# Performance work log

Hardware: AMD Instinct MI355X
Metric: run time of the kernel (lower is better)

## Reference

```python
import jax, jax.numpy as jnp
import numpy as np
import math

NO, NR, E = 100000, 1000, 1000000
DO, DR, DE, H, OM = 64, 32, 4, 64, 32


def setup_inputs() -> dict:
    key = jax.random.key(0)
    ks = jax.random.split(key, 20)
    s = lambda k, sh: jax.random.normal(k, sh, dtype=jnp.float32) * 0.05
    inp = {
        'x_order': jax.random.normal(ks[0], (NO, DO), dtype=jnp.float32),
        'x_rider': jax.random.normal(ks[1], (NR, DR), dtype=jnp.float32),
        'edge_attr': jax.random.normal(ks[2], (E, DE), dtype=jnp.float32),
        'order_idx': jax.random.randint(ks[3], (E,), 0, NO),
        'rider_idx': jax.random.randint(ks[4], (E,), 0, NR),
        'omega_encoded': jax.random.normal(ks[5], (OM,), dtype=jnp.float32),
        # TransformerConv params (heads=1)
        'Wk': s(ks[6], (DO, H)), 'bk': jnp.zeros((H,), jnp.float32),
        'Wq': s(ks[7], (DR, H)), 'bq': jnp.zeros((H,), jnp.float32),
        'Wv': s(ks[8], (DO, H)), 'bv': jnp.zeros((H,), jnp.float32),
        'We': s(ks[9], (DE, H)),  # lin_edge, bias=False in PyG
        'Wskip': s(ks[10], (DR, H)), 'bskip': jnp.zeros((H,), jnp.float32),
        # order_proj
        'Wp': s(ks[11], (DO, H)), 'bp': jnp.zeros((H,), jnp.float32),
        # residual MLP: Linear(2H+OM,128) -> ReLU -> Linear(128,1)
        'W1': s(ks[12], (2 * H + OM, 128)), 'b1': jnp.zeros((128,), jnp.float32),
        'W2': s(ks[13], (128, 1)), 'b2': jnp.zeros((1,), jnp.float32),
    }
    return inp


def _segment_softmax(alpha, seg, num_segments):
    m = jax.ops.segment_max(alpha, seg, num_segments=num_segments)
    m = jnp.where(jnp.isfinite(m), m, 0.0)
    ex = jnp.exp(alpha - m[seg])
    denom = jax.ops.segment_sum(ex, seg, num_segments=num_segments)
    return ex / (denom[seg] + 1e-16)


def reference(x_order, x_rider, edge_attr, order_idx, rider_idx, omega_encoded,
              Wk, bk, Wq, bq, Wv, bv, We, Wskip, bskip, Wp, bp, W1, b1, W2, b2):
    scale = 1.0 / math.sqrt(H)
    # TransformerConv((order, rider) -> rider), heads=1, edge_dim
    q = x_rider @ Wq + bq            # [NR, H]
    k = x_order @ Wk + bk            # [NO, H]
    v = x_order @ Wv + bv            # [NO, H]
    e = edge_attr @ We               # [E, H]
    k_j = k[order_idx] + e           # [E, H]
    v_j = v[order_idx] + e           # [E, H]
    alpha = jnp.sum(q[rider_idx] * k_j, axis=-1) * scale  # [E]
    alpha = _segment_softmax(alpha, rider_idx, NR)
    agg = jax.ops.segment_sum(alpha[:, None] * v_j, rider_idx, num_segments=NR)  # [NR, H]
    rider_emb = agg + x_rider @ Wskip + bskip  # root/skip connection

    # edge scoring
    order_proj = x_order @ Wp + bp   # [NO, H]
    oe = order_proj[order_idx]       # [E, H]
    re = rider_emb[rider_idx]        # [E, H]
    dot = jnp.sum(oe * re, axis=-1) * scale  # [E]
    omega_expand = jnp.broadcast_to(omega_encoded[None, :], (oe.shape[0], OM))
    resid_in = jnp.concatenate([oe, re, omega_expand], axis=-1)  # [E, 2H+OM]
    hmid = jax.nn.relu(resid_in @ W1 + b1)
    resid = (hmid @ W2 + b2)[:, 0]
    return jnp.clip(dot + resid, -10.0, 10.0)
```

## Files before the change

### kernel.cpp

```cpp
#include <hip/hip_runtime.h>
#include <hip/hip_bf16.h>
#include <math.h>
#include <stdint.h>

#define NO_N 100000
#define NR_N 1000
#define E_N  1000000
#define SB     250
#define SCHUNK 4000
#define KVP_TILES 1563
#define KVP_BLKS 1024
#define MAXTILES 17008

typedef short bf16x8 __attribute__((ext_vector_type(8)));
typedef float floatx4 __attribute__((ext_vector_type(4)));

__device__ __forceinline__ unsigned short bfu(float x) {
    union { __hip_bfloat16 h; unsigned short u; } c;
    c.h = __float2bfloat16(x);
    return c.u;
}
__device__ __forceinline__ float bflo(unsigned int u) {
    return __uint_as_float(u << 16);
}
__device__ __forceinline__ float bfhi(unsigned int u) {
    return __uint_as_float(u & 0xffff0000u);
}

__global__ __launch_bounds__(256) void k_front(
    const float* __restrict__ xr,
    const float* __restrict__ Wq, const float* __restrict__ bq,
    const float* __restrict__ Wskip, const float* __restrict__ bskip,
    const float* __restrict__ We,
    float* __restrict__ q, float* __restrict__ skip, float* __restrict__ t,
    const float* __restrict__ W1, const float* __restrict__ b1,
    const float* __restrict__ omega, float* __restrict__ b1eff,
    unsigned short* __restrict__ w1t,
    const float* __restrict__ x,
    const float* __restrict__ Wk, const float* __restrict__ bk,
    const float* __restrict__ Wv, const float* __restrict__ bv,
    const float* __restrict__ Wp, const float* __restrict__ bp,
    unsigned short* __restrict__ kb, unsigned short* __restrict__ vb,
    unsigned short* __restrict__ pb,
    const int* __restrict__ ridx, int* __restrict__ ghist)
{
    __shared__ __align__(16) char smem[9216];
    const int tid = threadIdx.x;
    const int b = blockIdx.x;

    if (b < 250) {
        float* sx = (float*)smem;
        float* sq = sx + 128;
        int rbase = b * 4;
        if (tid < 128) {
            int rl = tid >> 5, d = tid & 31;
            sx[rl * 32 + d] = xr[(rbase + rl) * 32 + d];
        }
        __syncthreads();
        int rl = tid >> 6, h = tid & 63;
        int r = rbase + rl;
        float aq = bq[h], as = bskip[h];
        #pragma unroll 4
        for (int d = 0; d < 32; ++d) {
            float xv = sx[rl * 32 + d];
            aq += xv * Wq[d * 64 + h];
            as += xv * Wskip[d * 64 + h];
        }
        sq[rl * 64 + h] = aq;
        q[r * 64 + h] = aq;
        skip[r * 64 + h] = as;
        __syncthreads();
        if (tid < 16) {
            int rl2 = tid >> 2, d = tid & 3;
            float acc = 0.f;
            for (int hh = 0; hh < 64; ++hh)
                acc += We[d * 64 + hh] * sq[rl2 * 64 + hh];
            t[(rbase + rl2) * 4 + d] = acc;
        }
    } else if (b == 250) {
        if (tid < 128) {
            float acc = b1[tid];
            #pragma unroll 4
            for (int j = 0; j < 32; ++j)
                acc += omega[j] * W1[(128 + j) * 128 + tid];
            b1eff[tid] = acc;
        }
        for (int idx = tid; idx < 64 * 128; idx += 256) {
            int n = idx >> 6, k = idx & 63;
            w1t[idx] = bfu(W1[k * 128 + n]);
        }
    } else if (b < 251 + KVP_BLKS) {
        unsigned short* sX = (unsigned short*)smem;
        const int wave = tid >> 6, lane = tid & 63;
        const int l15 = lane & 15, quad = lane >> 4;

        bf16x8 bfr[3][2];
        float bias[3];
        unsigned short* outT[3];
        int colc[3];
        #pragma unroll
        for (int ct = 0; ct < 3; ++ct) {
            int n = wave * 48 + ct * 16 + l15;
            int table = n >> 6, c = n & 63;
            const float* W  = (table == 0) ? Wk : (table == 1) ? Wv : Wp;
            const float* bb = (table == 0) ? bk : (table == 1) ? bv : bp;
            bias[ct] = bb[c];
            colc[ct] = c;
            outT[ct] = (table == 0) ? kb : (table == 1) ? vb : pb;
            #pragma unroll
            for (int kf = 0; kf < 2; ++kf) {
                bf16x8 f;
                #pragma unroll
                for (int j = 0; j < 8; ++j)
                    f[j] = (short)bfu(W[(size_t)(kf * 32 + quad * 8 + j) * 64 + c]);
                bfr[ct][kf] = f;
            }
        }

        const int srl = tid >> 2;
        const int sqt = (tid & 3) * 16;

        for (int tile = b - 251; tile < KVP_TILES; tile += KVP_BLKS) {
            int rowbase = tile * 64;
            {
                int row = rowbase + srl;
                unsigned short* dst = sX + srl * 72 + sqt;
                if (row < NO_N) {
                    const float4* src = (const float4*)(x + (size_t)row * 64 + sqt);
                    #pragma unroll
                    for (int i = 0; i < 4; ++i) {
                        float4 a = src[i];
                        ushort4 u = { bfu(a.x), bfu(a.y), bfu(a.z), bfu(a.w) };
                        *(ushort4*)(dst + i * 4) = u;
                    }
                } else {
                    ushort4 z = {0, 0, 0, 0};
                    #pragma unroll
                    for (int i = 0; i < 4; ++i) *(ushort4*)(dst + i * 4) = z;
                }
            }
            __syncthreads();

            floatx4 acc[4][3];
            #pragma unroll
            for (int rt = 0; rt < 4; ++rt)
                #pragma unroll
                for (int ct = 0; ct < 3; ++ct)
                    acc[rt][ct] = (floatx4){bias[ct], bias[ct], bias[ct], bias[ct]};

            #pragma unroll
            for (int rt = 0; rt < 4; ++rt) {
                const unsigned short* ar = sX + (size_t)(rt * 16 + l15) * 72 + quad * 8;
                bf16x8 a0 = *(const bf16x8*)(ar);
                bf16x8 a1 = *(const bf16x8*)(ar + 32);
                #pragma unroll
                for (int ct = 0; ct < 3; ++ct) {
                    floatx4 c = acc[rt][ct];
                    c = __builtin_amdgcn_mfma_f32_16x16x32_bf16(a0, bfr[ct][0], c, 0, 0, 0);
                    c = __builtin_amdgcn_mfma_f32_16x16x32_bf16(a1, bfr[ct][1], c, 0, 0, 0);
                    acc[rt][ct] = c;
                }
            }

            #pragma unroll
            for (int rt = 0; rt < 4; ++rt) {
                int rb = rowbase + rt * 16 + quad * 4;
                #pragma unroll
                for (int ct = 0; ct < 3; ++ct) {
                    unsigned short* o = outT[ct];
                    size_t cbase = colc[ct];
                    #pragma unroll
                    for (int g = 0; g < 4; ++g) {
                        int row = rb + g;
                        if (row < NO_N)
                            o[(size_t)row * 64 + cbase] = bfu(acc[rt][ct][g]);
                    }
                }
            }
            __syncthreads();
        }
    } else {
        int* hc = (int*)smem;
        int hb = b - (251 + KVP_BLKS);
        for (int i = tid; i < NR_N; i += 256) hc[i] = 0;
        __syncthreads();
        int s = hb * SCHUNK;
        for (int i = s + tid; i < s + SCHUNK; i += 256)
            atomicAdd(&hc[ridx[i]], 1);
        __syncthreads();
        for (int i = tid; i < NR_N; i += 256)
            ghist[i * SB + hb] = hc[i];
    }
}

__global__ __launch_bounds__(256) void k_colscan(const int* __restrict__ ghist,
                                                 int* __restrict__ gpre,
                                                 int* __restrict__ counts)
{
    __shared__ int s[256];
    int tid = threadIdx.x, r = blockIdx.x;
    int v = (tid < SB) ? ghist[r * SB + tid] : 0;
    s[tid] = v;
    __syncthreads();
    for (int off = 1; off < 256; off <<= 1) {
        int tv = (tid >= off) ? s[tid - off] : 0;
        __syncthreads();
        s[tid] += tv;
        __syncthreads();
    }
    if (tid < SB) gpre[r * SB + tid] = s[tid] - v;
    if (tid == 255) counts[r] = s[255];
}

__global__ __launch_bounds__(1024) void k_scan(const int* __restrict__ counts,
                                               int* __restrict__ offsets,
                                               int* __restrict__ tilestart)
{
    __shared__ int s[1024];
    int tid = threadIdx.x;
    int c = (tid < NR_N) ? counts[tid] : 0;
    s[tid] = c;
    __syncthreads();
    for (int off = 1; off < 1024; off <<= 1) {
        int tv = (tid >= off) ? s[tid - off] : 0;
        __syncthreads();
        s[tid] += tv;
        __syncthreads();
    }
    if (tid < NR_N) offsets[tid] = s[tid] - c;
    if (tid == NR_N - 1) offsets[NR_N] = s[tid];
    __syncthreads();
    int tc = (tid < NR_N) ? ((c + 63) >> 6) : 0;
    s[tid] = tc;
    __syncthreads();
    for (int off = 1; off < 1024; off <<= 1) {
        int tv = (tid >= off) ? s[tid - off] : 0;
        __syncthreads();
        s[tid] += tv;
        __syncthreads();
    }
    if (tid < NR_N) tilestart[tid] = s[tid] - tc;
    if (tid == NR_N - 1) tilestart[NR_N] = s[tid];
}

__global__ __launch_bounds__(256) void k_trec(const int* __restrict__ tilestart,
                                              const int* __restrict__ offsets,
                                              int4* __restrict__ trec)
{
    int nt = tilestart[NR_N];
    int t = blockIdx.x * 256 + threadIdx.x;
    if (t >= nt) return;
    int lo = 0, hi = NR_N - 1;
    while (lo < hi) {
        int mid = (lo + hi + 1) >> 1;
        if (tilestart[mid] <= t) lo = mid; else hi = mid - 1;
    }
    trec[t] = make_int4(lo, offsets[lo] + ((t - tilestart[lo]) << 6),
                        offsets[lo + 1], 0);
}

__global__ __launch_bounds__(1024) void k_scatter2(
    const int* __restrict__ ridx, const int* __restrict__ oidx,
    const float* __restrict__ ea, const float* __restrict__ t,
    const int* __restrict__ offsets, const int* __restrict__ gpre,
    int4* __restrict__ spack, int* __restrict__ so, int* __restrict__ rank)
{
    __shared__ int cur[NR_N];
    int tid = threadIdx.x, b = blockIdx.x;
    for (int i = tid; i < NR_N; i += 1024)
        cur[i] = offsets[i] + gpre[i * SB + b];
    __syncthreads();
    int s = b * SCHUNK;
    for (int i = s + tid; i < s + SCHUNK; i += 1024) {
        int r = ridx[i];
        int o = oidx[i];
        float4 e4 = *(const float4*)(ea + (size_t)i * 4);
        float4 t4 = *(const float4*)(t + r * 4);
        float h = e4.x * t4.x + e4.y * t4.y + e4.z * t4.z + e4.w * t4.w;
        int pos = atomicAdd(&cur[r], 1);
        int4 pk;
        pk.x = o;
        pk.y = __float_as_int(h);
        pk.z = (int)((unsigned)bfu(e4.x) | ((unsigned)bfu(e4.y) << 16));
        pk.w = (int)((unsigned)bfu(e4.z) | ((unsigned)bfu(e4.w) << 16));
        spack[pos] = pk;
        so[pos] = o;
        rank[i] = pos;
    }
}

__global__ __launch_bounds__(512) void k_rider(
    const int* __restrict__ offsets, const int4* __restrict__ spack,
    const float* __restrict__ q,
    const unsigned short* __restrict__ kb, const unsigned short* __restrict__ vb,
    const float* __restrict__ We, const float* __restrict__ skip,
    const float* __restrict__ W1, const float* __restrict__ b1eff,
    unsigned short* __restrict__ embb, float* __restrict__ Br)
{
    __shared__ float sQ[64];
    __shared__ int2 sOX[8][64];
    __shared__ float rv[8][64];
    __shared__ float re4[8][4];
    __shared__ float rd[8];

    int r = blockIdx.x;
    int wave = threadIdx.x >> 6, lane = threadIdx.x & 63;
    if (threadIdx.x < 64) sQ[threadIdx.x] = q[r * 64 + threadIdx.x];
    __syncthreads();

    int beg = offsets[r], end = offsets[r + 1];
    int cnt = end - beg;
    int chunk = (cnt + 7) >> 3;
    int s0 = beg + wave * chunk;
    int s1 = min(s0 + chunk, end);

    float aggv = 0.f, dsum = 0.f;
    float ag0 = 0.f, ag1 = 0.f, ag2 = 0.f, ag3 = 0.f;
    const float2* sQ2 = (const float2*)sQ;

    for (int jb = s0; jb < s1; jb += 64) {
        int j = jb + lane;
        bool valid = (j < s1);
        int4 pk = make_int4(0, 0, 0, 0);
        if (valid) pk = spack[j];
        int oo = pk.x;
        float h = __int_as_float(pk.y);

        const uint4* krow = (const uint4*)(kb + (size_t)oo * 64);
        uint4 K0 = krow[0], K1 = krow[1], K2 = krow[2], K3 = krow[3];
        uint4 K4 = krow[4], K5 = krow[5], K6 = krow[6], K7 = krow[7];
        float acc = h;
        #define DOT8(Kv, base) { \
            float2 qa = sQ2[(base) + 0]; \
            acc = fmaf(bflo(Kv.x), qa.x, acc); acc = fmaf(bfhi(Kv.x), qa.y, acc); \
            float2 qb = sQ2[(base) + 1]; \
            acc = fmaf(bflo(Kv.y), qb.x, acc); acc = fmaf(bfhi(Kv.y), qb.y, acc); \
            float2 qc = sQ2[(base) + 2]; \
            acc = fmaf(bflo(Kv.z), qc.x, acc); acc = fmaf(bfhi(Kv.z), qc.y, acc); \
            float2 qd = sQ2[(base) + 3]; \
            acc = fmaf(bflo(Kv.w), qd.x, acc); acc = fmaf(bfhi(Kv.w), qd.y, acc); }
        DOT8(K0, 0) DOT8(K1, 4) DOT8(K2, 8) DOT8(K3, 12)
        DOT8(K4, 16) DOT8(K5, 20) DOT8(K6, 24) DOT8(K7, 28)
        #undef DOT8

        float exv = valid ? __expf(acc * 0.125f) : 0.f;
        dsum += exv;
        unsigned int ez = (unsigned int)pk.z, ew = (unsigned int)pk.w;
        ag0 = fmaf(exv, bflo(ez), ag0);
        ag1 = fmaf(exv, bfhi(ez), ag1);
        ag2 = fmaf(exv, bflo(ew), ag2);
        ag3 = fmaf(exv, bfhi(ew), ag3);

        sOX[wave][lane] = make_int2(oo, __float_as_int(exv));

        int nn = min(s1 - jb, 64);
        int i = 0;
        for (; i + 8 <= nn; i += 8) {
            int2 x0 = sOX[wave][i + 0], x1 = sOX[wave][i + 1];
            int2 x2 = sOX[wave][i + 2], x3 = sOX[wave][i + 3];
            int2 x4 = sOX[wave][i + 4], x5 = sOX[wave][i + 5];
            int2 x6 = sOX[wave][i + 6], x7 = sOX[wave][i + 7];
            unsigned short u0 = vb[(size_t)x0.x * 64 + lane];
            unsigned short u1 = vb[(size_t)x1.x * 64 + lane];
            unsigned short u2 = vb[(size_t)x2.x * 64 + lane];
            unsigned short u3 = vb[(size_t)x3.x * 64 + lane];
            unsigned short u4 = vb[(size_t)x4.x * 64 + lane];
            unsigned short u5 = vb[(size_t)x5.x * 64 + lane];
            unsigned short u6 = vb[(size_t)x6.x * 64 + lane];
            unsigned short u7 = vb[(size_t)x7.x * 64 + lane];
            aggv = fmaf(__int_as_float(x0.y), __uint_as_float((unsigned int)u0 << 16), aggv);
            aggv = fmaf(__int_as_float(x1.y), __uint_as_float((unsigned int)u1 << 16), aggv);
            aggv = fmaf(__int_as_float(x2.y), __uint_as_float((unsigned int)u2 << 16), aggv);
            aggv = fmaf(__int_as_float(x3.y), __uint_as_float((unsigned int)u3 << 16), aggv);
            aggv = fmaf(__int_as_float(x4.y), __uint_as_float((unsigned int)u4 << 16), aggv);
            aggv = fmaf(__int_as_float(x5.y), __uint_as_float((unsigned int)u5 << 16), aggv);
            aggv = fmaf(__int_as_float(x6.y), __uint_as_float((unsigned int)u6 << 16), aggv);
            aggv = fmaf(__int_as_float(x7.y), __uint_as_float((unsigned int)u7 << 16), aggv);
        }
        for (; i < nn; ++i) {
            int2 xx = sOX[wave][i];
            unsigned short uu = vb[(size_t)xx.x * 64 + lane];
            aggv = fmaf(__int_as_float(xx.y), __uint_as_float((unsigned int)uu << 16), aggv);
        }
    }

    #pragma unroll
    for (int m = 1; m < 64; m <<= 1) {
        dsum += __shfl_xor(dsum, m);
        ag0 += __shfl_xor(ag0, m);
        ag1 += __shfl_xor(ag1, m);
        ag2 += __shfl_xor(ag2, m);
        ag3 += __shfl_xor(ag3, m);
    }

    rv[wave][lane] = aggv;
    if (lane == 0) {
        rd[wave] = dsum;
        re4[wave][0] = ag0; re4[wave][1] = ag1;
        re4[wave][2] = ag2; re4[wave][3] = ag3;
    }
    __syncthreads();
    if (threadIdx.x < 64) {
        int l = threadIdx.x;
        float av = 0.f, ds = 0.f, a0 = 0.f, a1 = 0.f, a2 = 0.f, a3 = 0.f;
        #pragma unroll
        for (int w = 0; w < 8; ++w) {
            av += rv[w][l]; ds += rd[w];
            a0 += re4[w][0]; a1 += re4[w][1]; a2 += re4[w][2]; a3 += re4[w][3];
        }
        float corr = a0 * We[0 * 64 + l] + a1 * We[1 * 64 + l]
                   + a2 * We[2 * 64 + l] + a3 * We[3 * 64 + l];
        float val = (av + corr) / (ds + 1e-16f) + skip[r * 64 + l];
        embb[r * 64 + l] = bfu(val);
        sQ[l] = val;
    }
    __syncthreads();
    if (threadIdx.x < 128) {
        int c = threadIdx.x;
        float a = b1eff[c];
        #pragma unroll 8
        for (int d = 0; d < 64; ++d)
            a = fmaf(sQ[d], W1[(size_t)(64 + d) * 128 + c], a);
        Br[r * 128 + c] = a;
    }
}

__global__ __launch_bounds__(256) void k_edge2(
    const int* __restrict__ so, const int4* __restrict__ trec,
    const int* __restrict__ tilestart,
    const unsigned short* __restrict__ pb, const unsigned short* __restrict__ embb,
    const float* __restrict__ Br, const unsigned short* __restrict__ w1t,
    const float* __restrict__ W2, const float* __restrict__ b2,
    float* __restrict__ tmp)
{
    const int tid = threadIdx.x;
    const int wave = tid >> 6;
    const int lane = tid & 63;
    const int l15 = lane & 15;
    const int quad = lane >> 4;

    bf16x8 bfr[8][2];
    floatx4 w2q[8];
    #pragma unroll
    for (int ctl = 0; ctl < 8; ++ctl) {
        int n = ctl * 16 + l15;
        bfr[ctl][0] = *(const bf16x8*)(w1t + n * 64 + quad * 8);
        bfr[ctl][1] = *(const bf16x8*)(w1t + n * 64 + 32 + quad * 8);
        w2q[ctl] = *(const floatx4*)(W2 + ctl * 16 + quad * 4);
    }
    float b2v = b2[0];
    const int ntiles = tilestart[NR_N];
    const bf16x8 z8 = (bf16x8){0, 0, 0, 0, 0, 0, 0, 0};

    union U4B { uint4 u; bf16x8 b; };

    const int stride = gridDim.x * 4;
    int tile = blockIdx.x * 4 + wave;
    if (tile >= ntiles) return;

    int4 rr = trec[tile];
    int o_rt[4];
    #pragma unroll
    for (int rt = 0; rt < 4; ++rt)
        o_rt[rt] = so[min(rr.y + rt * 16 + l15, rr.z - 1)];

    for (; tile < ntiles; tile += stride) {
        const int r = rr.x, jb = rr.y, jend = rr.z;

        U4B A0[4], A1[4];
        #pragma unroll
        for (int rt = 0; rt < 4; ++rt) {
            const unsigned short* rowp = pb + (size_t)o_rt[rt] * 64 + quad * 8;
            A0[rt].u = *(const uint4*)(rowp);
            A1[rt].u = *(const uint4*)(rowp + 32);
        }

        int4 rrn = trec[min(tile + stride, ntiles - 1)];
        int o_nx[4];
        #pragma unroll
        for (int rt = 0; rt < 4; ++rt)
            o_nx[rt] = so[min(rrn.y + rt * 16 + l15, rrn.z - 1)];

        const unsigned short* eb = embb + r * 64;
        bf16x8 b80 = z8, b81 = z8;
        if (l15 == 0) {
            b80 = *(const bf16x8*)(eb + quad * 8);
            b81 = *(const bf16x8*)(eb + 32 + quad * 8);
        }

        const float* brrow = Br + r * 128;

        #pragma unroll
        for (int rt = 0; rt < 4; ++rt) {
            float s = 0.f;
            #pragma unroll
            for (int ctl = 0; ctl < 8; ++ctl) {
                floatx4 c = *(const floatx4*)(brrow + ctl * 16 + quad * 4);
                c = __builtin_amdgcn_mfma_f32_16x16x32_bf16(bfr[ctl][0], A0[rt].b, c, 0, 0, 0);
                c = __builtin_amdgcn_mfma_f32_16x16x32_bf16(bfr[ctl][1], A1[rt].b, c, 0, 0, 0);
                #pragma unroll
                for (int g = 0; g < 4; ++g)
                    s = fmaf(fmaxf(c[g], 0.f), w2q[ctl][g], s);
            }
            floatx4 c8 = (floatx4){0.f, 0.f, 0.f, 0.f};
            c8 = __builtin_amdgcn_mfma_f32_16x16x32_bf16(b80, A0[rt].b, c8, 0, 0, 0);
            c8 = __builtin_amdgcn_mfma_f32_16x16x32_bf16(b81, A1[rt].b, c8, 0, 0, 0);

            s += __shfl_xor(s, 16);
            s += __shfl_xor(s, 32);

            if (quad == 0) {
                int pos = jb + rt * 16 + l15;
                if (pos < jend) {
                    float v = s + 0.125f * c8[0] + b2v;
                    tmp[pos] = fminf(fmaxf(v, -10.f), 10.f);
                }
            }
        }

        rr = rrn;
        #pragma unroll
        for (int rt = 0; rt < 4; ++rt) o_rt[rt] = o_nx[rt];
    }
}

__global__ __launch_bounds__(256) void k_perm(const int* __restrict__ rank,
                                              const float* __restrict__ tmp,
                                              float* __restrict__ out)
{
    int i = blockIdx.x * 256 + threadIdx.x;
    if (i < E_N) out[i] = tmp[rank[i]];
}

extern "C" void kernel_launch(void* const* d_in, const int* in_sizes, int n_in,
                              void* d_out, int out_size, void* d_ws, size_t ws_size,
                              hipStream_t stream)
{
    const float* x_order   = (const float*)d_in[0];
    const float* x_rider   = (const float*)d_in[1];
    const float* edge_attr = (const float*)d_in[2];
    const int*   order_idx = (const int*)d_in[3];
    const int*   rider_idx = (const int*)d_in[4];
    const float* omega     = (const float*)d_in[5];
    const float* Wk = (const float*)d_in[6];  const float* bk = (const float*)d_in[7];
    const float* Wq = (const float*)d_in[8];  const float* bq = (const float*)d_in[9];
    const float* Wv = (const float*)d_in[10]; const float* bv = (const float*)d_in[11];
    const float* We = (const float*)d_in[12];
    const float* Wskip = (const float*)d_in[13]; const float* bskip = (const float*)d_in[14];
    const float* Wp = (const float*)d_in[15]; const float* bp = (const float*)d_in[16];
    const float* W1 = (const float*)d_in[17]; const float* b1 = (const float*)d_in[18];
    const float* W2 = (const float*)d_in[19]; const float* b2 = (const float*)d_in[20];
    float* out = (float*)d_out;

    unsigned short* ws_kb = (unsigned short*)d_ws;
    unsigned short* ws_vb = ws_kb + (size_t)NO_N * 64;
    unsigned short* ws_pb = ws_vb + (size_t)NO_N * 64;
    int4* ws_spack = (int4*)(ws_pb + (size_t)NO_N * 64);
    float* ws_tmp  = (float*)ws_spack;
    int*  ws_so    = (int*)(ws_spack + E_N);
    int*  ws_rank  = ws_so + E_N;
    float* wsf     = (float*)(ws_rank + E_N);
    float* ws_q    = wsf;
    float* ws_skip = ws_q + NR_N * 64;
    unsigned short* ws_embb = (unsigned short*)(ws_skip + NR_N * 64);
    float* ws_t    = (float*)(ws_embb + NR_N * 64);
    float* ws_b1e  = ws_t + NR_N * 4;
    unsigned short* ws_w1t = (unsigned short*)(ws_b1e + 128);
    float* ws_Br   = (float*)(ws_w1t + 128 * 64);
    int* ws_counts  = (int*)(ws_Br + NR_N * 128);
    int* ws_offsets = ws_counts + NR_N;
    int* ws_tilest  = ws_offsets + NR_N + 8;
    int* ws_ghist   = ws_tilest + NR_N + 8;
    int* ws_gpre    = ws_ghist + NR_N * SB;
    int4* ws_trec   = (int4*)(((uintptr_t)(ws_gpre + NR_N * SB) + 15) & ~(uintptr_t)15);

    k_front<<<251 + KVP_BLKS + SB, 256, 0, stream>>>(
        x_rider, Wq, bq, Wskip, bskip, We, ws_q, ws_skip, ws_t,
        W1, b1, omega, ws_b1e, ws_w1t,
        x_order, Wk, bk, Wv, bv, Wp, bp, ws_kb, ws_vb, ws_pb,
        rider_idx, ws_ghist);
    k_colscan<<<NR_N, 256, 0, stream>>>(ws_ghist, ws_gpre, ws_counts);
    k_scan<<<1, 1024, 0, stream>>>(ws_counts, ws_offsets, ws_tilest);
    k_trec<<<(MAXTILES + 255) / 256, 256, 0, stream>>>(ws_tilest, ws_offsets, ws_trec);
    k_scatter2<<<SB, 1024, 0, stream>>>(rider_idx, order_idx, edge_attr, ws_t,
                                        ws_offsets, ws_gpre, ws_spack, ws_so, ws_rank);
    k_rider<<<NR_N, 512, 0, stream>>>(ws_offsets, ws_spack, ws_q,
                                      ws_kb, ws_vb, We, ws_skip,
                                      W1, ws_b1e, ws_embb, ws_Br);
    k_edge2<<<1024, 256, 0, stream>>>(ws_so, ws_trec, ws_tilest,
                                      ws_pb, ws_embb, ws_Br, ws_w1t, W2, b2, ws_tmp);
    k_perm<<<(E_N + 255) / 256, 256, 0, stream>>>(ws_rank, ws_tmp, out);
}
```

Baseline: 281.7 us.

## Stage scatter output in shared memory, grouped by rider, before global writes

```diff
diff --git a/kernel.cpp b/kernel.cpp
--- a/kernel.cpp
+++ b/kernel.cpp
@@ -263,13 +263,34 @@
     const int* __restrict__ ridx, const int* __restrict__ oidx,
     const float* __restrict__ ea, const float* __restrict__ t,
     const int* __restrict__ offsets, const int* __restrict__ gpre,
+    const int* __restrict__ ghist,
     int4* __restrict__ spack, int* __restrict__ so, int* __restrict__ rank)
 {
-    __shared__ int cur[NR_N];
-    int tid = threadIdx.x, b = blockIdx.x;
-    for (int i = tid; i < NR_N; i += 1024)
-        cur[i] = offsets[i] + gpre[i * SB + b];
-    __syncthreads();
+    __shared__ int stmp[1024];
+    __shared__ int lpre[NR_N];
+    __shared__ int lcur[NR_N];
+    __shared__ int gbase[NR_N];
+    __shared__ __align__(16) int4 sbuf[SCHUNK];
+    __shared__ int spos[SCHUNK];
+
+    const int tid = threadIdx.x, b = blockIdx.x;
+
+    int v = (tid < NR_N) ? ghist[tid * SB + b] : 0;
+    stmp[tid] = v;
+    __syncthreads();
+    for (int off = 1; off < 1024; off <<= 1) {
+        int tv = (tid >= off) ? stmp[tid - off] : 0;
+        __syncthreads();
+        stmp[tid] += tv;
+        __syncthreads();
+    }
+    if (tid < NR_N) {
+        lpre[tid] = stmp[tid] - v;
+        lcur[tid] = 0;
+        gbase[tid] = offsets[tid] + gpre[tid * SB + b];
+    }
+    __syncthreads();
+
     int s = b * SCHUNK;
     for (int i = s + tid; i < s + SCHUNK; i += 1024) {
         int r = ridx[i];
@@ -277,15 +298,25 @@
         float4 e4 = *(const float4*)(ea + (size_t)i * 4);
         float4 t4 = *(const float4*)(t + r * 4);
         float h = e4.x * t4.x + e4.y * t4.y + e4.z * t4.z + e4.w * t4.w;
-        int pos = atomicAdd(&cur[r], 1);
+        int old = atomicAdd(&lcur[r], 1);
+        int lpos = lpre[r] + old;
+        int gp = gbase[r] + old;
         int4 pk;
         pk.x = o;
         pk.y = __float_as_int(h);
         pk.z = (int)((unsigned)bfu(e4.x) | ((unsigned)bfu(e4.y) << 16));
         pk.w = (int)((unsigned)bfu(e4.z) | ((unsigned)bfu(e4.w) << 16));
-        spack[pos] = pk;
-        so[pos] = o;
-        rank[i] = pos;
+        sbuf[lpos] = pk;
+        spos[lpos] = gp;
+        rank[i] = gp;
+    }
+    __syncthreads();
+
+    for (int l = tid; l < SCHUNK; l += 1024) {
+        int4 pk = sbuf[l];
+        int gp = spos[l];
+        spack[gp] = pk;
+        so[gp] = pk.x;
     }
 }
 
@@ -583,7 +614,8 @@
     k_scan<<<1, 1024, 0, stream>>>(ws_counts, ws_offsets, ws_tilest);
     k_trec<<<(MAXTILES + 255) / 256, 256, 0, stream>>>(ws_tilest, ws_offsets, ws_trec);
     k_scatter2<<<SB, 1024, 0, stream>>>(rider_idx, order_idx, edge_attr, ws_t,
-                                        ws_offsets, ws_gpre, ws_spack, ws_so, ws_rank);
+                                        ws_offsets, ws_gpre, ws_ghist,
+                                        ws_spack, ws_so, ws_rank);
     k_rider<<<NR_N, 512, 0, stream>>>(ws_offsets, ws_spack, ws_q,
                                       ws_kb, ws_vb, We, ws_skip,
                                       W1, ws_b1e, ws_embb, ws_Br);
```

Result: faster. 271.4 us (-3.7%).

## Move K/V/P projection into scatter kernel and split dot-product accumulators

Applied to the files above, without the earlier changes.

```diff
diff --git a/kernel.cpp b/kernel.cpp
--- a/kernel.cpp
+++ b/kernel.cpp
@@ -36,15 +36,9 @@
     const float* __restrict__ W1, const float* __restrict__ b1,
     const float* __restrict__ omega, float* __restrict__ b1eff,
     unsigned short* __restrict__ w1t,
-    const float* __restrict__ x,
-    const float* __restrict__ Wk, const float* __restrict__ bk,
-    const float* __restrict__ Wv, const float* __restrict__ bv,
-    const float* __restrict__ Wp, const float* __restrict__ bp,
-    unsigned short* __restrict__ kb, unsigned short* __restrict__ vb,
-    unsigned short* __restrict__ pb,
     const int* __restrict__ ridx, int* __restrict__ ghist)
 {
-    __shared__ __align__(16) char smem[9216];
+    __shared__ __align__(16) char smem[4096];
     const int tid = threadIdx.x;
     const int b = blockIdx.x;
 
@@ -89,7 +83,125 @@
             int n = idx >> 6, k = idx & 63;
             w1t[idx] = bfu(W1[k * 128 + n]);
         }
-    } else if (b < 251 + KVP_BLKS) {
+    } else {
+        int* hc = (int*)smem;
+        int hb = b - 251;
+        for (int i = tid; i < NR_N; i += 256) hc[i] = 0;
+        __syncthreads();
+        int s = hb * SCHUNK;
+        for (int i = s + tid; i < s + SCHUNK; i += 256)
+            atomicAdd(&hc[ridx[i]], 1);
+        __syncthreads();
+        for (int i = tid; i < NR_N; i += 256)
+            ghist[i * SB + hb] = hc[i];
+    }
+}
+
+__global__ __launch_bounds__(256) void k_colscan(const int* __restrict__ ghist,
+                                                 int* __restrict__ gpre,
+                                                 int* __restrict__ counts)
+{
+    __shared__ int s[256];
+    int tid = threadIdx.x, r = blockIdx.x;
+    int v = (tid < SB) ? ghist[r * SB + tid] : 0;
+    s[tid] = v;
+    __syncthreads();
+    for (int off = 1; off < 256; off <<= 1) {
+        int tv = (tid >= off) ? s[tid - off] : 0;
+        __syncthreads();
+        s[tid] += tv;
+        __syncthreads();
+    }
+    if (tid < SB) gpre[r * SB + tid] = s[tid] - v;
+    if (tid == 255) counts[r] = s[255];
+}
+
+__global__ __launch_bounds__(1024) void k_scan(const int* __restrict__ counts,
+                                               int* __restrict__ offsets,
+                                               int* __restrict__ tilestart)
+{
+    __shared__ int s[1024];
+    int tid = threadIdx.x;
+    int c = (tid < NR_N) ? counts[tid] : 0;
+    s[tid] = c;
+    __syncthreads();
+    for (int off = 1; off < 1024; off <<= 1) {
+        int tv = (tid >= off) ? s[tid - off] : 0;
+        __syncthreads();
+        s[tid] += tv;
+        __syncthreads();
+    }
+    if (tid < NR_N) offsets[tid] = s[tid] - c;
+    if (tid == NR_N - 1) offsets[NR_N] = s[tid];
+    __syncthreads();
+    int tc = (tid < NR_N) ? ((c + 63) >> 6) : 0;
+    s[tid] = tc;
+    __syncthreads();
+    for (int off = 1; off < 1024; off <<= 1) {
+        int tv = (tid >= off) ? s[tid - off] : 0;
+        __syncthreads();
+        s[tid] += tv;
+        __syncthreads();
+    }
+    if (tid < NR_N) tilestart[tid] = s[tid] - tc;
+    if (tid == NR_N - 1) tilestart[NR_N] = s[tid];
+}
+
+__global__ __launch_bounds__(256) void k_trec(const int* __restrict__ tilestart,
+                                              const int* __restrict__ offsets,
+                                              int4* __restrict__ trec)
+{
+    int nt = tilestart[NR_N];
+    int t = blockIdx.x * 256 + threadIdx.x;
+    if (t >= nt) return;
+    int lo = 0, hi = NR_N - 1;
+    while (lo < hi) {
+        int mid = (lo + hi + 1) >> 1;
+        if (tilestart[mid] <= t) lo = mid; else hi = mid - 1;
+    }
+    trec[t] = make_int4(lo, offsets[lo] + ((t - tilestart[lo]) << 6),
+                        offsets[lo + 1], 0);
+}
+
+__global__ __launch_bounds__(256) void k_scatkvp(
+    const int* __restrict__ ridx, const int* __restrict__ oidx,
+    const float* __restrict__ ea, const float* __restrict__ t,
+    const int* __restrict__ offsets, const int* __restrict__ gpre,
+    int4* __restrict__ spack, int* __restrict__ so, int* __restrict__ rank,
+    const float* __restrict__ x,
+    const float* __restrict__ Wk, const float* __restrict__ bk,
+    const float* __restrict__ Wv, const float* __restrict__ bv,
+    const float* __restrict__ Wp, const float* __restrict__ bp,
+    unsigned short* __restrict__ kb, unsigned short* __restrict__ vb,
+    unsigned short* __restrict__ pb)
+{
+    __shared__ __align__(16) char smem[9216];
+    const int tid = threadIdx.x;
+    const int b = blockIdx.x;
+
+    if (b < SB) {
+        int* cur = (int*)smem;
+        for (int i = tid; i < NR_N; i += 256)
+            cur[i] = offsets[i] + gpre[i * SB + b];
+        __syncthreads();
+        int s = b * SCHUNK;
+        for (int i = s + tid; i < s + SCHUNK; i += 256) {
+            int r = ridx[i];
+            int o = oidx[i];
+            float4 e4 = *(const float4*)(ea + (size_t)i * 4);
+            float4 t4 = *(const float4*)(t + r * 4);
+            float h = e4.x * t4.x + e4.y * t4.y + e4.z * t4.z + e4.w * t4.w;
+            int pos = atomicAdd(&cur[r], 1);
+            int4 pk;
+            pk.x = o;
+            pk.y = __float_as_int(h);
+            pk.z = (int)((unsigned)bfu(e4.x) | ((unsigned)bfu(e4.y) << 16));
+            pk.w = (int)((unsigned)bfu(e4.z) | ((unsigned)bfu(e4.w) << 16));
+            spack[pos] = pk;
+            so[pos] = o;
+            rank[i] = pos;
+        }
+    } else {
         unsigned short* sX = (unsigned short*)smem;
         const int wave = tid >> 6, lane = tid & 63;
         const int l15 = lane & 15, quad = lane >> 4;
@@ -120,7 +232,7 @@
         const int srl = tid >> 2;
         const int sqt = (tid & 3) * 16;
 
-        for (int tile = b - 251; tile < KVP_TILES; tile += KVP_BLKS) {
+        for (int tile = b - SB; tile < KVP_TILES; tile += KVP_BLKS) {
             int rowbase = tile * 64;
             {
                 int row = rowbase + srl;
@@ -179,113 +291,6 @@
             }
             __syncthreads();
         }
-    } else {
-        int* hc = (int*)smem;
-        int hb = b - (251 + KVP_BLKS);
-        for (int i = tid; i < NR_N; i += 256) hc[i] = 0;
-        __syncthreads();
-        int s = hb * SCHUNK;
-        for (int i = s + tid; i < s + SCHUNK; i += 256)
-            atomicAdd(&hc[ridx[i]], 1);
-        __syncthreads();
-        for (int i = tid; i < NR_N; i += 256)
-            ghist[i * SB + hb] = hc[i];
-    }
-}
-
-__global__ __launch_bounds__(256) void k_colscan(const int* __restrict__ ghist,
-                                                 int* __restrict__ gpre,
-                                                 int* __restrict__ counts)
-{
-    __shared__ int s[256];
-    int tid = threadIdx.x, r = blockIdx.x;
-    int v = (tid < SB) ? ghist[r * SB + tid] : 0;
-    s[tid] = v;
-    __syncthreads();
-    for (int off = 1; off < 256; off <<= 1) {
-        int tv = (tid >= off) ? s[tid - off] : 0;
-        __syncthreads();
-        s[tid] += tv;
-        __syncthreads();
-    }
-    if (tid < SB) gpre[r * SB + tid] = s[tid] - v;
-    if (tid == 255) counts[r] = s[255];
-}
-
-__global__ __launch_bounds__(1024) void k_scan(const int* __restrict__ counts,
-                                               int* __restrict__ offsets,
-                                               int* __restrict__ tilestart)
-{
-    __shared__ int s[1024];
-    int tid = threadIdx.x;
-    int c = (tid < NR_N) ? counts[tid] : 0;
-    s[tid] = c;
-    __syncthreads();
-    for (int off = 1; off < 1024; off <<= 1) {
-        int tv = (tid >= off) ? s[tid - off] : 0;
-        __syncthreads();
-        s[tid] += tv;
-        __syncthreads();
-    }
-    if (tid < NR_N) offsets[tid] = s[tid] - c;
-    if (tid == NR_N - 1) offsets[NR_N] = s[tid];
-    __syncthreads();
-    int tc = (tid < NR_N) ? ((c + 63) >> 6) : 0;
-    s[tid] = tc;
-    __syncthreads();
-    for (int off = 1; off < 1024; off <<= 1) {
-        int tv = (tid >= off) ? s[tid - off] : 0;
-        __syncthreads();
-        s[tid] += tv;
-        __syncthreads();
-    }
-    if (tid < NR_N) tilestart[tid] = s[tid] - tc;
-    if (tid == NR_N - 1) tilestart[NR_N] = s[tid];
-}
-
-__global__ __launch_bounds__(256) void k_trec(const int* __restrict__ tilestart,
-                                              const int* __restrict__ offsets,
-                                              int4* __restrict__ trec)
-{
-    int nt = tilestart[NR_N];
-    int t = blockIdx.x * 256 + threadIdx.x;
-    if (t >= nt) return;
-    int lo = 0, hi = NR_N - 1;
-    while (lo < hi) {
-        int mid = (lo + hi + 1) >> 1;
-        if (tilestart[mid] <= t) lo = mid; else hi = mid - 1;
-    }
-    trec[t] = make_int4(lo, offsets[lo] + ((t - tilestart[lo]) << 6),
-                        offsets[lo + 1], 0);
-}
-
-__global__ __launch_bounds__(1024) void k_scatter2(
-    const int* __restrict__ ridx, const int* __restrict__ oidx,
-    const float* __restrict__ ea, const float* __restrict__ t,
-    const int* __restrict__ offsets, const int* __restrict__ gpre,
-    int4* __restrict__ spack, int* __restrict__ so, int* __restrict__ rank)
-{
-    __shared__ int cur[NR_N];
-    int tid = threadIdx.x, b = blockIdx.x;
-    for (int i = tid; i < NR_N; i += 1024)
-        cur[i] = offsets[i] + gpre[i * SB + b];
-    __syncthreads();
-    int s = b * SCHUNK;
-    for (int i = s + tid; i < s + SCHUNK; i += 1024) {
-        int r = ridx[i];
-        int o = oidx[i];
-        float4 e4 = *(const float4*)(ea + (size_t)i * 4);
-        float4 t4 = *(const float4*)(t + r * 4);
-        float h = e4.x * t4.x + e4.y * t4.y + e4.z * t4.z + e4.w * t4.w;
-        int pos = atomicAdd(&cur[r], 1);
-        int4 pk;
-        pk.x = o;
-        pk.y = __float_as_int(h);
-        pk.z = (int)((unsigned)bfu(e4.x) | ((unsigned)bfu(e4.y) << 16));
-        pk.w = (int)((unsigned)bfu(e4.z) | ((unsigned)bfu(e4.w) << 16));
-        spack[pos] = pk;
-        so[pos] = o;
-        rank[i] = pos;
     }
 }
 
@@ -314,7 +319,8 @@
     int s0 = beg + wave * chunk;
     int s1 = min(s0 + chunk, end);
 
-    float aggv = 0.f, dsum = 0.f;
+    float av0 = 0.f, av1 = 0.f, av2 = 0.f, av3 = 0.f;
+    float dsum = 0.f;
     float ag0 = 0.f, ag1 = 0.f, ag2 = 0.f, ag3 = 0.f;
     const float2* sQ2 = (const float2*)sQ;
 
@@ -329,19 +335,20 @@
         const uint4* krow = (const uint4*)(kb + (size_t)oo * 64);
         uint4 K0 = krow[0], K1 = krow[1], K2 = krow[2], K3 = krow[3];
         uint4 K4 = krow[4], K5 = krow[5], K6 = krow[6], K7 = krow[7];
-        float acc = h;
-        #define DOT8(Kv, base) { \
+        float a0 = h, a1 = 0.f, a2 = 0.f, a3 = 0.f;
+        #define DOT8(Kv, base, A) { \
             float2 qa = sQ2[(base) + 0]; \
-            acc = fmaf(bflo(Kv.x), qa.x, acc); acc = fmaf(bfhi(Kv.x), qa.y, acc); \
+            A = fmaf(bflo(Kv.x), qa.x, A); A = fmaf(bfhi(Kv.x), qa.y, A); \
             float2 qb = sQ2[(base) + 1]; \
-            acc = fmaf(bflo(Kv.y), qb.x, acc); acc = fmaf(bfhi(Kv.y), qb.y, acc); \
+            A = fmaf(bflo(Kv.y), qb.x, A); A = fmaf(bfhi(Kv.y), qb.y, A); \
             float2 qc = sQ2[(base) + 2]; \
-            acc = fmaf(bflo(Kv.z), qc.x, acc); acc = fmaf(bfhi(Kv.z), qc.y, acc); \
+            A = fmaf(bflo(Kv.z), qc.x, A); A = fmaf(bfhi(Kv.z), qc.y, A); \
             float2 qd = sQ2[(base) + 3]; \
-            acc = fmaf(bflo(Kv.w), qd.x, acc); acc = fmaf(bfhi(Kv.w), qd.y, acc); }
-        DOT8(K0, 0) DOT8(K1, 4) DOT8(K2, 8) DOT8(K3, 12)
-        DOT8(K4, 16) DOT8(K5, 20) DOT8(K6, 24) DOT8(K7, 28)
+            A = fmaf(bflo(Kv.w), qd.x, A); A = fmaf(bfhi(Kv.w), qd.y, A); }
+        DOT8(K0, 0, a0) DOT8(K1, 4, a1) DOT8(K2, 8, a2) DOT8(K3, 12, a3)
+        DOT8(K4, 16, a0) DOT8(K5, 20, a1) DOT8(K6, 24, a2) DOT8(K7, 28, a3)
         #undef DOT8
+        float acc = (a0 + a1) + (a2 + a3);
 
         float exv = valid ? __expf(acc * 0.125f) : 0.f;
         dsum += exv;
@@ -368,21 +375,23 @@
             unsigned short u5 = vb[(size_t)x5.x * 64 + lane];
             unsigned short u6 = vb[(size_t)x6.x * 64 + lane];
             unsigned short u7 = vb[(size_t)x7.x * 64 + lane];
-            aggv = fmaf(__int_as_float(x0.y), __uint_as_float((unsigned int)u0 << 16), aggv);
-            aggv = fmaf(__int_as_float(x1.y), __uint_as_float((unsigned int)u1 << 16), aggv);
-            aggv = fmaf(__int_as_float(x2.y), __uint_as_float((unsigned int)u2 << 16), aggv);
-            aggv = fmaf(__int_as_float(x3.y), __uint_as_float((unsigned int)u3 << 16), aggv);
-            aggv = fmaf(__int_as_float(x4.y), __uint_as_float((unsigned int)u4 << 16), aggv);
-            aggv = fmaf(__int_as_float(x5.y), __uint_as_float((unsigned int)u5 << 16), aggv);
-            aggv = fmaf(__int_as_float(x6.y), __uint_as_float((unsigned int)u6 << 16), aggv);
-            aggv = fmaf(__int_as_float(x7.y), __uint_as_float((unsigned int)u7 << 16), aggv);
+            av0 = fmaf(__int_as_float(x0.y), __uint_as_float((unsigned int)u0 << 16), av0);
+            av1 = fmaf(__int_as_float(x1.y), __uint_as_float((unsigned int)u1 << 16), av1);
+            av2 = fmaf(__int_as_float(x2.y), __uint_as_float((unsigned int)u2 << 16), av2);
+            av3 = fmaf(__int_as_float(x3.y), __uint_as_float((unsigned int)u3 << 16), av3);
+            av0 = fmaf(__int_as_float(x4.y), __uint_as_float((unsigned int)u4 << 16), av0);
+            av1 = fmaf(__int_as_float(x5.y), __uint_as_float((unsigned int)u5 << 16), av1);
+            av2 = fmaf(__int_as_float(x6.y), __uint_as_float((unsigned int)u6 << 16), av2);
+            av3 = fmaf(__int_as_float(x7.y), __uint_as_float((unsigned int)u7 << 16), av3);
         }
         for (; i < nn; ++i) {
             int2 xx = sOX[wave][i];
             unsigned short uu = vb[(size_t)xx.x * 64 + lane];
-            aggv = fmaf(__int_as_float(xx.y), __uint_as_float((unsigned int)uu << 16), aggv);
-        }
-    }
+            av0 = fmaf(__int_as_float(xx.y), __uint_as_float((unsigned int)uu << 16), av0);
+        }
+    }
+
+    float aggv = (av0 + av1) + (av2 + av3);
 
     #pragma unroll
     for (int m = 1; m < 64; m <<= 1) {
@@ -574,16 +583,17 @@
     int* ws_gpre    = ws_ghist + NR_N * SB;
     int4* ws_trec   = (int4*)(((uintptr_t)(ws_gpre + NR_N * SB) + 15) & ~(uintptr_t)15);
 
-    k_front<<<251 + KVP_BLKS + SB, 256, 0, stream>>>(
+    k_front<<<251 + SB, 256, 0, stream>>>(
         x_rider, Wq, bq, Wskip, bskip, We, ws_q, ws_skip, ws_t,
         W1, b1, omega, ws_b1e, ws_w1t,
-        x_order, Wk, bk, Wv, bv, Wp, bp, ws_kb, ws_vb, ws_pb,
         rider_idx, ws_ghist);
     k_colscan<<<NR_N, 256, 0, stream>>>(ws_ghist, ws_gpre, ws_counts);
     k_scan<<<1, 1024, 0, stream>>>(ws_counts, ws_offsets, ws_tilest);
     k_trec<<<(MAXTILES + 255) / 256, 256, 0, stream>>>(ws_tilest, ws_offsets, ws_trec);
-    k_scatter2<<<SB, 1024, 0, stream>>>(rider_idx, order_idx, edge_attr, ws_t,
-                                        ws_offsets, ws_gpre, ws_spack, ws_so, ws_rank);
+    k_scatkvp<<<SB + KVP_BLKS, 256, 0, stream>>>(
+        rider_idx, order_idx, edge_attr, ws_t,
+        ws_offsets, ws_gpre, ws_spack, ws_so, ws_rank,
+        x_order, Wk, bk, Wv, bv, Wp, bp, ws_kb, ws_vb, ws_pb);
     k_rider<<<NR_N, 512, 0, stream>>>(ws_offsets, ws_spack, ws_q,
                                       ws_kb, ws_vb, We, ws_skip,
                                       W1, ws_b1e, ws_embb, ws_Br);
```

Measured after the change: 279.8 us. Within noise of the previous version (-0.7%).
